# Optimization experiments

Measured on AMD Instinct MI355X. Metric: run time of the kernel, lower is better.

Reference implementation:

```python
import jax, jax.numpy as jnp
import numpy as np

B, C, P, D = 4096, 1000, 10, 256
N = C * P            # total prototypes
E = 160000           # edges among prototypes
MARGIN = -0.1
LOSS_WEIGHT = 0.1
EPS = 1e-12          # F.normalize eps


def _gcn_conv(x, src, dst, deg_isqrt, w, b):
    # PyG GCNConv: symmetric-normalized aggregation with self-loops (added by caller)
    xw = x @ w                                   # [N, D]
    norm = deg_isqrt[src] * deg_isqrt[dst]       # [E+N]
    msg = norm[:, None] * xw[src]                # [E+N, D]
    out = jax.ops.segment_sum(msg, dst, num_segments=N)
    return out + b


def setup_inputs() -> dict:
    key = jax.random.key(0)
    ks = jax.random.split(key, 8)
    return {
        "hidden": jax.random.normal(ks[0], (B, D), jnp.float32),
        "labels": jax.random.randint(ks[1], (B,), 0, C),
        "edge_index": jax.random.randint(ks[2], (2, E), 0, N),
        "node_features": 0.02 * jax.random.normal(ks[3], (N, D), jnp.float32),
        "w1": jax.random.normal(ks[4], (D, D), jnp.float32) / np.sqrt(D),
        "b1": jnp.zeros((D,), jnp.float32),
        "w2": jax.random.normal(ks[5], (D, D), jnp.float32) / np.sqrt(D),
        "b2": jnp.zeros((D,), jnp.float32),
    }


def reference(hidden, labels, edge_index, node_features, w1, b1, w2, b2):
    # --- PrototypeGCN over the prototype graph (self-loops + sym norm) ---
    loops = jnp.arange(N, dtype=edge_index.dtype)
    src = jnp.concatenate([edge_index[0], loops])
    dst = jnp.concatenate([edge_index[1], loops])
    deg = jax.ops.segment_sum(jnp.ones_like(dst, jnp.float32), dst, num_segments=N)
    deg_isqrt = jnp.where(deg > 0, jax.lax.rsqrt(jnp.maximum(deg, 1.0)), 0.0)
    x = node_features
    x = jax.nn.relu(_gcn_conv(x, src, dst, deg_isqrt, w1, b1))
    x = jax.nn.relu(_gcn_conv(x, src, dst, deg_isqrt, w2, b2))

    # --- cosine similarity, per-class max over prototypes ---
    hidden_norm = hidden / jnp.maximum(jnp.linalg.norm(hidden, axis=1, keepdims=True), EPS)
    proto_norm = x / jnp.maximum(jnp.linalg.norm(x, axis=1, keepdims=True), EPS)
    sim = (1.0 + hidden_norm @ proto_norm.T) / 2.0          # [B, N]
    sim_pc = sim.reshape(B, C, P)
    output = sim_pc.max(axis=2)                              # [B, C]
    topk_idx = sim_pc.argmax(axis=2)                         # [B, C]

    # --- margin-masked cross entropy ---
    ar = jnp.arange(B)
    true_scores = output[ar, labels]
    pred_labels = output.argmax(axis=1)
    pred_scores = output.max(axis=1)
    mask = (true_scores - pred_scores) > MARGIN              # [B] bool
    cnt = mask.sum()
    per_ce = -jax.nn.log_softmax(output, axis=1)[ar, labels]
    ce_loss = jnp.sum(per_ce * mask) / jnp.maximum(cnt, 1).astype(per_ce.dtype)

    # dispersion = -mean(proto_norm @ proto_norm.T) = -||sum_i p_i||^2 / N^2
    s = proto_norm.sum(axis=0)
    dispersion_loss = -(s @ s) / (N * N)
    total_loss = jnp.where(cnt == 0, 0.0, ce_loss + LOSS_WEIGHT * dispersion_loss)

    # --- vectorized usage scatter (replaces Python double loop) ---
    pos_ids = labels * P + topk_idx[ar, labels]
    positive_usage = jnp.zeros((N,), jnp.float32).at[pos_ids].add(1.0)
    wrong = (pred_labels != labels).astype(jnp.float32)
    neg_ids = pred_labels * P + topk_idx[ar, pred_labels]
    negative_usage = jnp.zeros((N,), jnp.float32).at[neg_ids].add(wrong)

    return (output, total_loss, positive_usage, negative_usage)
```

## Files before the change

kernel.cpp:

```cpp
#include <hip/hip_runtime.h>
#include <math.h>

#define B_  4096
#define C_  1000
#define P_  10
#define D_  256
#define N_  10000
#define E_  160000

typedef __attribute__((ext_vector_type(8))) short short8;
typedef __attribute__((ext_vector_type(4))) float floatx4;

#define MFMA16(a, b, c) __builtin_amdgcn_mfma_f32_16x16x32_bf16((a), (b), (c), 0, 0, 0)

__device__ __forceinline__ float waveReduceSum(float v){
  #pragma unroll
  for (int o = 32; o > 0; o >>= 1) v += __shfl_xor(v, o);
  return v;
}
__device__ __forceinline__ unsigned short f2bf(float f){
  unsigned int u = __float_as_uint(f);
  unsigned int r = (u + 0x7FFFu + ((u >> 16) & 1u)) >> 16;
  return (unsigned short)r;
}
__device__ __forceinline__ float bf2f(unsigned short b){
  return __uint_as_float(((unsigned int)b) << 16);
}
__device__ __forceinline__ void gload_lds16(const void* g, void* l){
  __builtin_amdgcn_global_load_lds((const __attribute__((address_space(1))) void*)g,
                                   (__attribute__((address_space(3))) void*)l, 16, 0, 0);
}

__global__ void k_prep(const int* __restrict__ src, const int* __restrict__ dst,
                       int* __restrict__ cursor, int* __restrict__ csr_src,
                       const float* __restrict__ w1, const float* __restrict__ w2,
                       unsigned short* __restrict__ w1h, unsigned short* __restrict__ w1l,
                       unsigned short* __restrict__ w2h, unsigned short* __restrict__ w2l,
                       float* __restrict__ zero_zone,
                       const float* __restrict__ nodef,
                       unsigned short* __restrict__ NFh, unsigned short* __restrict__ NFl,
                       const float* __restrict__ hidden,
                       unsigned short* __restrict__ HNh, unsigned short* __restrict__ HNl){
  int b = blockIdx.x;
  int t = threadIdx.x;
  if (b < 625){
    int e = b * 256 + t;
    if (e < E_){
      int d = dst[e];
      int p = atomicAdd(&cursor[d], 1);
      p = (p < 63) ? p : 63;
      csr_src[d * 64 + p] = src[e];
    }
  } else if (b < 1137){
    int bb = b - 625;
    const float* w = (bb < 256) ? w1 : w2;
    int n = bb & 255;
    float x = w[(size_t)t * 256 + n];
    unsigned short h = f2bf(x);
    unsigned short l = f2bf(x - bf2f(h));
    if (bb < 256){ w1h[(size_t)n * 256 + t] = h; w1l[(size_t)n * 256 + t] = l; }
    else         { w2h[(size_t)n * 256 + t] = h; w2l[(size_t)n * 256 + t] = l; }
  } else if (b < 1216){
    int i = (b - 1137) * 256 + t;
    if (i < 1 + 2 * N_) zero_zone[i] = 0.f;
  } else if (b < 11216){
    size_t i = (size_t)(b - 1216) * 256 + t;
    float x = nodef[i];
    unsigned short h = f2bf(x);
    NFh[i] = h;
    NFl[i] = f2bf(x - bf2f(h));
  } else {
    int r = b - 11216;
    float v = hidden[(size_t)r * 256 + t];
    float ss = waveReduceSum(v * v);
    __shared__ float red[4];
    int w = t >> 6;
    if ((t & 63) == 0) red[w] = ss;
    __syncthreads();
    float tot = red[0] + red[1] + red[2] + red[3];
    float nrm = fmaxf(sqrtf(tot), 1e-12f);
    float x = v / nrm;
    unsigned short h = f2bf(x);
    HNh[(size_t)r * 256 + t] = h;
    HNl[(size_t)r * 256 + t] = f2bf(x - bf2f(h));
  }
}

__global__ __launch_bounds__(64) void k_gemm_mfma(
    const unsigned short* __restrict__ Ah, const unsigned short* __restrict__ Al,
    const unsigned short* __restrict__ Wh, const unsigned short* __restrict__ Wl,
    float* __restrict__ outp){
  int lane = threadIdx.x;
  int l15 = lane & 15, lq = lane >> 4;
  int rb = blockIdx.x * 64;
  int nb = blockIdx.y * 32;

  floatx4 acc[4][2];
  #pragma unroll
  for (int mt = 0; mt < 4; ++mt)
    #pragma unroll
    for (int nt = 0; nt < 2; ++nt) acc[mt][nt] = (floatx4){0.f,0.f,0.f,0.f};

  int arow[4];
  #pragma unroll
  for (int mt = 0; mt < 4; ++mt){
    int r = rb + mt * 16 + l15;
    arow[mt] = (r < N_) ? r : (N_ - 1);
  }
  for (int kc = 0; kc < 256; kc += 32){
    short8 ah[4], al[4], bh[2], bl[2];
    #pragma unroll
    for (int mt = 0; mt < 4; ++mt){
      size_t o = (size_t)arow[mt] * 256 + kc + lq * 8;
      ah[mt] = *(const short8*)(Ah + o);
      al[mt] = *(const short8*)(Al + o);
    }
    #pragma unroll
    for (int nt = 0; nt < 2; ++nt){
      size_t o = (size_t)(nb + nt * 16 + l15) * 256 + kc + lq * 8;
      bh[nt] = *(const short8*)(Wh + o);
      bl[nt] = *(const short8*)(Wl + o);
    }
    #pragma unroll
    for (int nt = 0; nt < 2; ++nt)
      #pragma unroll
      for (int mt = 0; mt < 4; ++mt) acc[mt][nt] = MFMA16(al[mt], bh[nt], acc[mt][nt]);
    #pragma unroll
    for (int nt = 0; nt < 2; ++nt)
      #pragma unroll
      for (int mt = 0; mt < 4; ++mt) acc[mt][nt] = MFMA16(ah[mt], bl[nt], acc[mt][nt]);
    #pragma unroll
    for (int nt = 0; nt < 2; ++nt)
      #pragma unroll
      for (int mt = 0; mt < 4; ++mt) acc[mt][nt] = MFMA16(ah[mt], bh[nt], acc[mt][nt]);
  }
  #pragma unroll
  for (int mt = 0; mt < 4; ++mt)
    #pragma unroll
    for (int r = 0; r < 4; ++r){
      int row = rb + mt * 16 + lq * 4 + r;
      if (row < N_){
        #pragma unroll
        for (int nt = 0; nt < 2; ++nt)
          outp[(size_t)row * 256 + nb + nt * 16 + l15] = acc[mt][nt][r];
      }
    }
}

__global__ void k_agg_split(const float* __restrict__ XW, const int* __restrict__ deg,
                            const int* __restrict__ csr_src,
                            const float* __restrict__ bias,
                            unsigned short* __restrict__ Xh, unsigned short* __restrict__ Xl){
  int n    = blockIdx.x * 4 + (threadIdx.x >> 6);
  int lane = threadIdx.x & 63;
  int c4   = lane * 4;
  int dgn = deg[n];
  int dg = (dgn < 64) ? dgn : 64;
  int   esr = (lane < dg) ? csr_src[n * 64 + lane] : 0;
  float is  = 1.0f / sqrtf((float)(dgn + 1));
  float en  = (1.0f / sqrtf((float)(deg[esr] + 1))) * is;
  float4 s = *(const float4*)(XW + (size_t)n * 256 + c4);
  float w = is * is;
  float4 a = make_float4(w * s.x, w * s.y, w * s.z, w * s.w);
  int i = 0;
  for (; i + 3 < dg; i += 4){
    int s0 = __shfl(esr, i),   s1 = __shfl(esr, i+1), s2 = __shfl(esr, i+2), s3 = __shfl(esr, i+3);
    float n0 = __shfl(en, i),  n1 = __shfl(en, i+1),  n2 = __shfl(en, i+2),  n3 = __shfl(en, i+3);
    float4 v0 = *(const float4*)(XW + (size_t)s0 * 256 + c4);
    float4 v1 = *(const float4*)(XW + (size_t)s1 * 256 + c4);
    float4 v2 = *(const float4*)(XW + (size_t)s2 * 256 + c4);
    float4 v3 = *(const float4*)(XW + (size_t)s3 * 256 + c4);
    a.x += n0*v0.x + n1*v1.x + n2*v2.x + n3*v3.x;
    a.y += n0*v0.y + n1*v1.y + n2*v2.y + n3*v3.y;
    a.z += n0*v0.z + n1*v1.z + n2*v2.z + n3*v3.z;
    a.w += n0*v0.w + n1*v1.w + n2*v2.w + n3*v3.w;
  }
  for (; i < dg; ++i){
    int s0 = __shfl(esr, i); float n0 = __shfl(en, i);
    float4 v0 = *(const float4*)(XW + (size_t)s0 * 256 + c4);
    a.x += n0 * v0.x; a.y += n0 * v0.y; a.z += n0 * v0.z; a.w += n0 * v0.w;
  }
  float4 b = *(const float4*)(bias + c4);
  float x0 = fmaxf(a.x + b.x, 0.f), x1 = fmaxf(a.y + b.y, 0.f);
  float x2 = fmaxf(a.z + b.z, 0.f), x3 = fmaxf(a.w + b.w, 0.f);
  unsigned short h0 = f2bf(x0), h1 = f2bf(x1), h2 = f2bf(x2), h3 = f2bf(x3);
  ushort4 hv = make_ushort4(h0, h1, h2, h3);
  ushort4 lv = make_ushort4(f2bf(x0 - bf2f(h0)), f2bf(x1 - bf2f(h1)),
                            f2bf(x2 - bf2f(h2)), f2bf(x3 - bf2f(h3)));
  *(ushort4*)(Xh + (size_t)n * 256 + c4) = hv;
  *(ushort4*)(Xl + (size_t)n * 256 + c4) = lv;
}

__global__ void k_agg_norm_split(const float* __restrict__ XW, const int* __restrict__ deg,
                                 const int* __restrict__ csr_src,
                                 const float* __restrict__ bias,
                                 unsigned short* __restrict__ Ph, unsigned short* __restrict__ Pl){
  int n    = blockIdx.x * 4 + (threadIdx.x >> 6);
  int lane = threadIdx.x & 63;
  int c4   = lane * 4;
  int dgn = deg[n];
  int dg = (dgn < 64) ? dgn : 64;
  int   esr = (lane < dg) ? csr_src[n * 64 + lane] : 0;
  float is  = 1.0f / sqrtf((float)(dgn + 1));
  float en  = (1.0f / sqrtf((float)(deg[esr] + 1))) * is;
  float4 s = *(const float4*)(XW + (size_t)n * 256 + c4);
  float w = is * is;
  float4 a = make_float4(w * s.x, w * s.y, w * s.z, w * s.w);
  int i = 0;
  for (; i + 3 < dg; i += 4){
    int s0 = __shfl(esr, i),   s1 = __shfl(esr, i+1), s2 = __shfl(esr, i+2), s3 = __shfl(esr, i+3);
    float n0 = __shfl(en, i),  n1 = __shfl(en, i+1),  n2 = __shfl(en, i+2),  n3 = __shfl(en, i+3);
    float4 v0 = *(const float4*)(XW + (size_t)s0 * 256 + c4);
    float4 v1 = *(const float4*)(XW + (size_t)s1 * 256 + c4);
    float4 v2 = *(const float4*)(XW + (size_t)s2 * 256 + c4);
    float4 v3 = *(const float4*)(XW + (size_t)s3 * 256 + c4);
    a.x += n0*v0.x + n1*v1.x + n2*v2.x + n3*v3.x;
    a.y += n0*v0.y + n1*v1.y + n2*v2.y + n3*v3.y;
    a.z += n0*v0.z + n1*v1.z + n2*v2.z + n3*v3.z;
    a.w += n0*v0.w + n1*v1.w + n2*v2.w + n3*v3.w;
  }
  for (; i < dg; ++i){
    int s0 = __shfl(esr, i); float n0 = __shfl(en, i);
    float4 v0 = *(const float4*)(XW + (size_t)s0 * 256 + c4);
    a.x += n0 * v0.x; a.y += n0 * v0.y; a.z += n0 * v0.z; a.w += n0 * v0.w;
  }
  float4 b = *(const float4*)(bias + c4);
  float x0 = fmaxf(a.x + b.x, 0.f), x1 = fmaxf(a.y + b.y, 0.f);
  float x2 = fmaxf(a.z + b.z, 0.f), x3 = fmaxf(a.w + b.w, 0.f);
  float ss = x0*x0 + x1*x1 + x2*x2 + x3*x3;
  float tot = waveReduceSum(ss);
  float nrm = fmaxf(sqrtf(tot), 1e-12f);
  x0 /= nrm; x1 /= nrm; x2 /= nrm; x3 /= nrm;
  unsigned short h0 = f2bf(x0), h1 = f2bf(x1), h2 = f2bf(x2), h3 = f2bf(x3);
  ushort4 hv = make_ushort4(h0, h1, h2, h3);
  ushort4 lv = make_ushort4(f2bf(x0 - bf2f(h0)), f2bf(x1 - bf2f(h1)),
                            f2bf(x2 - bf2f(h2)), f2bf(x3 - bf2f(h3)));
  *(ushort4*)(Ph + (size_t)n * 256 + c4) = hv;
  *(ushort4*)(Pl + (size_t)n * 256 + c4) = lv;
}

__global__ __launch_bounds__(256, 4) void k_sim_max(
    const unsigned short* __restrict__ HNh, const unsigned short* __restrict__ HNl,
    const unsigned short* __restrict__ PNh, const unsigned short* __restrict__ PNl,
    float* __restrict__ out, unsigned char* __restrict__ idxb){
  __shared__ __align__(16) char smem[20736];

  int tid  = threadIdx.x;
  int wid  = tid >> 6;
  int lane = tid & 63;
  int l15  = lane & 15, lq = lane >> 4;
  int rbw  = blockIdx.y * 128 + wid * 32;
  int cb80 = blockIdx.x * 80;

  int swz  = (l15 >> 1) & 3;
  int srow = lane >> 2;
  int skq  = (lane & 3) ^ ((lane >> 3) & 3);

  floatx4 acc[2][5];
  #pragma unroll
  for (int mt = 0; mt < 2; ++mt)
    #pragma unroll
    for (int nt = 0; nt < 5; ++nt) acc[mt][nt] = (floatx4){0.f,0.f,0.f,0.f};

  const unsigned short* a0h = HNh + (size_t)(rbw + l15) * 256 + lq * 8;
  const unsigned short* a0l = HNl + (size_t)(rbw + l15) * 256 + lq * 8;

  auto stage1 = [&](int kc, int pb, int c){
    int bsel = (c >= 5) ? 1 : 0;
    int s = c - bsel * 5;
    int row = s * 16 + srow;
    const unsigned short* gp = (bsel ? PNl : PNh)
        + (size_t)(cb80 + row) * 256 + kc + skq * 8;
    char* lp = smem + pb * 10240 + bsel * 5120 + s * 1024;
    gload_lds16(gp, lp);
  };
  auto stageAll = [&](int kc, int pb){
    stage1(kc, pb, wid);
    stage1(kc, pb, wid + 4);
    if (wid < 2) stage1(kc, pb, wid + 8);
  };

  stageAll(0, 0);
  short8 ah[2], al[2];
  #pragma unroll
  for (int mt = 0; mt < 2; ++mt){
    ah[mt] = *(const short8*)(a0h + (size_t)mt * 4096);
    al[mt] = *(const short8*)(a0l + (size_t)mt * 4096);
  }
  __syncthreads();

  int p = 0;
  for (int kc = 0; kc < 256; kc += 32){
    const unsigned short* Bh = (const unsigned short*)(smem + p * 10240);
    const unsigned short* Bl = Bh + 2560;
    short8 ah2[2], al2[2];
    if (kc < 224){
      stageAll(kc + 32, p ^ 1);
      #pragma unroll
      for (int mt = 0; mt < 2; ++mt){
        ah2[mt] = *(const short8*)(a0h + (size_t)mt * 4096 + kc + 32);
        al2[mt] = *(const short8*)(a0l + (size_t)mt * 4096 + kc + 32);
      }
    }
    {
      int r0 = (0 * 16 + l15) * 32 + (lq ^ swz) * 8;
      int r1 = (1 * 16 + l15) * 32 + (lq ^ swz) * 8;
      int r2 = (2 * 16 + l15) * 32 + (lq ^ swz) * 8;
      short8 bh0 = *(const short8*)(Bh + r0), bl0 = *(const short8*)(Bl + r0);
      short8 bh1 = *(const short8*)(Bh + r1), bl1 = *(const short8*)(Bl + r1);
      short8 bh2 = *(const short8*)(Bh + r2), bl2 = *(const short8*)(Bl + r2);
      acc[0][0] = MFMA16(al[0], bh0, acc[0][0]);
      acc[1][0] = MFMA16(al[1], bh0, acc[1][0]);
      acc[0][1] = MFMA16(al[0], bh1, acc[0][1]);
      acc[1][1] = MFMA16(al[1], bh1, acc[1][1]);
      acc[0][2] = MFMA16(al[0], bh2, acc[0][2]);
      acc[1][2] = MFMA16(al[1], bh2, acc[1][2]);
      acc[0][0] = MFMA16(ah[0], bl0, acc[0][0]);
      acc[1][0] = MFMA16(ah[1], bl0, acc[1][0]);
      acc[0][1] = MFMA16(ah[0], bl1, acc[0][1]);
      acc[1][1] = MFMA16(ah[1], bl1, acc[1][1]);
      acc[0][2] = MFMA16(ah[0], bl2, acc[0][2]);
      acc[1][2] = MFMA16(ah[1], bl2, acc[1][2]);
      acc[0][0] = MFMA16(ah[0], bh0, acc[0][0]);
      acc[1][0] = MFMA16(ah[1], bh0, acc[1][0]);
      acc[0][1] = MFMA16(ah[0], bh1, acc[0][1]);
      acc[1][1] = MFMA16(ah[1], bh1, acc[1][1]);
      acc[0][2] = MFMA16(ah[0], bh2, acc[0][2]);
      acc[1][2] = MFMA16(ah[1], bh2, acc[1][2]);
    }
    {
      int r3 = (3 * 16 + l15) * 32 + (lq ^ swz) * 8;
      int r4 = (4 * 16 + l15) * 32 + (lq ^ swz) * 8;
      short8 bh3 = *(const short8*)(Bh + r3), bl3 = *(const short8*)(Bl + r3);
      short8 bh4 = *(const short8*)(Bh + r4), bl4 = *(const short8*)(Bl + r4);
      acc[0][3] = MFMA16(al[0], bh3, acc[0][3]);
      acc[1][3] = MFMA16(al[1], bh3, acc[1][3]);
      acc[0][4] = MFMA16(al[0], bh4, acc[0][4]);
      acc[1][4] = MFMA16(al[1], bh4, acc[1][4]);
      acc[0][3] = MFMA16(ah[0], bl3, acc[0][3]);
      acc[1][3] = MFMA16(ah[1], bl3, acc[1][3]);
      acc[0][4] = MFMA16(ah[0], bl4, acc[0][4]);
      acc[1][4] = MFMA16(ah[1], bl4, acc[1][4]);
      acc[0][3] = MFMA16(ah[0], bh3, acc[0][3]);
      acc[1][3] = MFMA16(ah[1], bh3, acc[1][3]);
      acc[0][4] = MFMA16(ah[0], bh4, acc[0][4]);
      acc[1][4] = MFMA16(ah[1], bh4, acc[1][4]);
    }
    ah[0] = ah2[0]; ah[1] = ah2[1];
    al[0] = al2[0]; al[1] = al2[1];
    __syncthreads();
    p ^= 1;
  }

  float* redw = (float*)smem + wid * 1296;
  #pragma unroll
  for (int mt = 0; mt < 2; ++mt){
    #pragma unroll
    for (int nt = 0; nt < 5; ++nt)
      #pragma unroll
      for (int r = 0; r < 4; ++r)
        redw[(lq * 4 + r) * 81 + nt * 16 + l15] = acc[mt][nt][r];
    int row = lane >> 2;
    int q   = lane & 3;
    const float* basep = redw + row * 81 + q * 20;
    float vs[2]; int is[2];
    #pragma unroll
    for (int cc = 0; cc < 2; ++cc){
      float m = 0.5f * (1.0f + basep[cc * 10]); int mi = 0;
      #pragma unroll
      for (int p2 = 1; p2 < 10; ++p2){
        float v = 0.5f * (1.0f + basep[cc * 10 + p2]);
        if (v > m){ m = v; mi = p2; }
      }
      vs[cc] = m; is[cc] = mi;
    }
    int grow = rbw + mt * 16 + row;
    int gcol = blockIdx.x * 8 + q * 2;
    *(float2*)(out + (size_t)grow * 1000 + gcol) = make_float2(vs[0], vs[1]);
    idxb[(size_t)grow * 1000 + gcol]     = (unsigned char)is[0];
    idxb[(size_t)grow * 1000 + gcol + 1] = (unsigned char)is[1];
  }
}

__global__ void k_row_pass(const float* __restrict__ out, const unsigned char* __restrict__ idxb,
                           const int* __restrict__ labels, int* __restrict__ cnt,
                           float* __restrict__ ce_sum, float* __restrict__ pos_usage,
                           float* __restrict__ neg_usage,
                           const unsigned short* __restrict__ Ph,
                           const unsigned short* __restrict__ Pl,
                           float* __restrict__ svec, int* __restrict__ done,
                           float* __restrict__ loss_out){
  int blk = blockIdx.x;
  if (blk < 1024){
    int b = blk * 4 + (threadIdx.x >> 6);
    int lane = threadIdx.x & 63;
    const float* row = out + (size_t)b * 1000;
    float m = -INFINITY, s = 0.f; int bi = 0x7fffffff;
    for (int c = lane; c < 1000; c += 64){
      float v = row[c];
      if (v > m){ s = s * expf(m - v) + 1.f; bi = c; m = v; }
      else       s += expf(v - m);
    }
    #pragma unroll
    for (int o = 32; o > 0; o >>= 1){
      float m2 = __shfl_xor(m, o);
      float s2 = __shfl_xor(s, o);
      int   b2 = __shfl_xor(bi, o);
      float M = fmaxf(m, m2);
      s = s * expf(m - M) + s2 * expf(m2 - M);
      if (m2 > m || (m2 == m && b2 < bi)) bi = b2;
      m = M;
    }
    if (lane == 0){
      int lab = labels[b];
      float true_score = row[lab];
      float per_ce = m + logf(s) - true_score;
      bool mask = (true_score - m) > -0.1f;
      if (mask){ atomicAdd(cnt, 1); atomicAdd(ce_sum, per_ce); }
      int pi = idxb[(size_t)b * 1000 + lab];
      atomicAdd(&pos_usage[lab * P_ + pi], 1.f);
      if (bi != lab){
        int ni = idxb[(size_t)b * 1000 + bi];
        atomicAdd(&neg_usage[bi * P_ + ni], 1.f);
      }
    }
  } else {
    int t = threadIdx.x;
    int r0 = (blk - 1024) * 100;
    float acc = 0.f;
    for (int rr = r0; rr < r0 + 100; ++rr)
      acc += bf2f(Ph[(size_t)rr * 256 + t]) + bf2f(Pl[(size_t)rr * 256 + t]);
    atomicAdd(&svec[t], acc);
  }
  __threadfence();
  __syncthreads();
  __shared__ int last;
  if (threadIdx.x == 0){
    int d = atomicAdd(done, 1);
    last = (d == 1124 - 1) ? 1 : 0;
  }
  __syncthreads();
  if (last){
    __threadfence();
    int t = threadIdx.x;
    float v = atomicAdd(&svec[t], 0.f);
    float ss = waveReduceSum(v * v);
    __shared__ float red[4];
    if ((t & 63) == 0) red[t >> 6] = ss;
    __syncthreads();
    if (t == 0){
      float tot = red[0] + red[1] + red[2] + red[3];
      float disp = -tot / 1.0e8f;
      int c = atomicAdd(cnt, 0);
      float ces = atomicAdd(ce_sum, 0.f);
      float total = (c == 0) ? 0.f
                  : (ces / (float)(c < 1 ? 1 : c) + 0.1f * disp);
      *loss_out = total;
    }
  }
}

extern "C" void kernel_launch(void* const* d_in, const int* in_sizes, int n_in,
                              void* d_out, int out_size, void* d_ws, size_t ws_size,
                              hipStream_t stream){
  const float* hidden = (const float*)d_in[0];
  const int*   labels = (const int*)  d_in[1];
  const int*   eidx   = (const int*)  d_in[2];
  const float* nodef  = (const float*)d_in[3];
  const float* w1     = (const float*)d_in[4];
  const float* b1     = (const float*)d_in[5];
  const float* w2     = (const float*)d_in[6];
  const float* b2     = (const float*)d_in[7];

  float* out       = (float*)d_out;
  float* loss_out  = out + (size_t)B_ * C_;
  float* pos_usage = loss_out + 1;
  float* neg_usage = pos_usage + N_;

  const int* srcp = eidx;
  const int* dstp = eidx + E_;

  char* base = (char*)d_ws;
  size_t off = 0;
  auto alloc = [&](size_t bytes) -> char* {
    char* p = base + off;
    off = (off + bytes + 255) & ~(size_t)255;
    return p;
  };
  int*   cursor  = (int*)  alloc((size_t)N_ * 4);
  float* svec    = (float*)alloc(256 * 4);
  int*   cnt     = (int*)  alloc(4);
  float* ce_sum  = (float*)alloc(4);
  int*   done    = (int*)  alloc(4);
  size_t zero_bytes = off;
  int*   csr_src   = (int*)  alloc((size_t)N_ * 64 * 4);
  float* XW        = (float*)alloc((size_t)N_ * 256 * 4);
  unsigned short* NFh = (unsigned short*)alloc((size_t)N_ * 256 * 2);
  unsigned short* NFl = (unsigned short*)alloc((size_t)N_ * 256 * 2);
  unsigned short* Xh  = (unsigned short*)alloc((size_t)N_ * 256 * 2);
  unsigned short* Xl  = (unsigned short*)alloc((size_t)N_ * 256 * 2);
  unsigned short* Ph  = (unsigned short*)alloc((size_t)N_ * 256 * 2);
  unsigned short* Pl  = (unsigned short*)alloc((size_t)N_ * 256 * 2);
  unsigned short* W1h = (unsigned short*)alloc(256 * 256 * 2);
  unsigned short* W1l = (unsigned short*)alloc(256 * 256 * 2);
  unsigned short* W2h = (unsigned short*)alloc(256 * 256 * 2);
  unsigned short* W2l = (unsigned short*)alloc(256 * 256 * 2);
  unsigned short* HNh = (unsigned short*)alloc((size_t)B_ * 256 * 2);
  unsigned short* HNl = (unsigned short*)alloc((size_t)B_ * 256 * 2);
  unsigned char* idxb = (unsigned char*)alloc((size_t)B_ * C_);

  hipMemsetAsync(base, 0, zero_bytes, stream);

  k_prep<<<15312, 256, 0, stream>>>(srcp, dstp, cursor, csr_src,
                                    w1, w2, W1h, W1l, W2h, W2l, loss_out,
                                    nodef, NFh, NFl, hidden, HNh, HNl);

  dim3 ggrid(157, 8);
  k_gemm_mfma<<<ggrid, 64, 0, stream>>>(NFh, NFl, W1h, W1l, XW);
  k_agg_split<<<N_ / 4, 256, 0, stream>>>(XW, cursor, csr_src, b1, Xh, Xl);
  k_gemm_mfma<<<ggrid, 64, 0, stream>>>(Xh, Xl, W2h, W2l, XW);
  k_agg_norm_split<<<N_ / 4, 256, 0, stream>>>(XW, cursor, csr_src, b2, Ph, Pl);

  dim3 sgrid(125, 32);
  k_sim_max<<<sgrid, 256, 0, stream>>>(HNh, HNl, Ph, Pl, out, idxb);

  k_row_pass<<<1124, 256, 0, stream>>>(out, idxb, labels, cnt, ce_sum,
                                       pos_usage, neg_usage, Ph, Pl, svec, done, loss_out);
}
```

Baseline: 383.3 us.

## Split row pass: separate colsum and finalize kernels, vectorize row max/softmax

Moves the prototype column-sum into its own kernel launched before the similarity kernel. Replaces the last-block completion counter with a separate single-block finalize kernel. Rewrites the per-row pass to load the row with float4 into registers, find max/argmax first, then compute the exp sum with fast intrinsics instead of the serial online softmax. Adds two kernel launches, and the fast exp/log intrinsics may slightly change numerics.

```diff
diff --git a/kernel.cpp b/kernel.cpp
--- a/kernel.cpp
+++ b/kernel.cpp
@@ -239,6 +239,17 @@
   *(ushort4*)(Pl + (size_t)n * 256 + c4) = lv;
 }
 
+__global__ void k_colsum(const unsigned short* __restrict__ hi,
+                         const unsigned short* __restrict__ lo,
+                         float* __restrict__ s){
+  int d = threadIdx.x;
+  int r0 = blockIdx.x * 100;
+  float acc = 0.f;
+  for (int r = r0; r < r0 + 100; ++r)
+    acc += bf2f(hi[(size_t)r * 256 + d]) + bf2f(lo[(size_t)r * 256 + d]);
+  atomicAdd(&s[d], acc);
+}
+
 __global__ __launch_bounds__(256, 4) void k_sim_max(
     const unsigned short* __restrict__ HNh, const unsigned short* __restrict__ HNl,
     const unsigned short* __restrict__ PNh, const unsigned short* __restrict__ PNl,
@@ -385,78 +396,69 @@
 __global__ void k_row_pass(const float* __restrict__ out, const unsigned char* __restrict__ idxb,
                            const int* __restrict__ labels, int* __restrict__ cnt,
                            float* __restrict__ ce_sum, float* __restrict__ pos_usage,
-                           float* __restrict__ neg_usage,
-                           const unsigned short* __restrict__ Ph,
-                           const unsigned short* __restrict__ Pl,
-                           float* __restrict__ svec, int* __restrict__ done,
-                           float* __restrict__ loss_out){
-  int blk = blockIdx.x;
-  if (blk < 1024){
-    int b = blk * 4 + (threadIdx.x >> 6);
-    int lane = threadIdx.x & 63;
-    const float* row = out + (size_t)b * 1000;
-    float m = -INFINITY, s = 0.f; int bi = 0x7fffffff;
-    for (int c = lane; c < 1000; c += 64){
-      float v = row[c];
-      if (v > m){ s = s * expf(m - v) + 1.f; bi = c; m = v; }
-      else       s += expf(v - m);
-    }
-    #pragma unroll
-    for (int o = 32; o > 0; o >>= 1){
-      float m2 = __shfl_xor(m, o);
-      float s2 = __shfl_xor(s, o);
-      int   b2 = __shfl_xor(bi, o);
-      float M = fmaxf(m, m2);
-      s = s * expf(m - M) + s2 * expf(m2 - M);
-      if (m2 > m || (m2 == m && b2 < bi)) bi = b2;
-      m = M;
-    }
-    if (lane == 0){
-      int lab = labels[b];
-      float true_score = row[lab];
-      float per_ce = m + logf(s) - true_score;
-      bool mask = (true_score - m) > -0.1f;
-      if (mask){ atomicAdd(cnt, 1); atomicAdd(ce_sum, per_ce); }
-      int pi = idxb[(size_t)b * 1000 + lab];
-      atomicAdd(&pos_usage[lab * P_ + pi], 1.f);
-      if (bi != lab){
-        int ni = idxb[(size_t)b * 1000 + bi];
-        atomicAdd(&neg_usage[bi * P_ + ni], 1.f);
-      }
-    }
-  } else {
-    int t = threadIdx.x;
-    int r0 = (blk - 1024) * 100;
-    float acc = 0.f;
-    for (int rr = r0; rr < r0 + 100; ++rr)
-      acc += bf2f(Ph[(size_t)rr * 256 + t]) + bf2f(Pl[(size_t)rr * 256 + t]);
-    atomicAdd(&svec[t], acc);
-  }
-  __threadfence();
+                           float* __restrict__ neg_usage){
+  int b = blockIdx.x * 4 + (threadIdx.x >> 6);
+  int lane = threadIdx.x & 63;
+  const float* row = out + (size_t)b * 1000;
+  float v[16];
+  #pragma unroll
+  for (int j = 0; j < 4; ++j){
+    int f4 = j * 64 + lane;
+    if (f4 < 250){
+      float4 t = *(const float4*)(row + f4 * 4);
+      v[j*4+0] = t.x; v[j*4+1] = t.y; v[j*4+2] = t.z; v[j*4+3] = t.w;
+    } else {
+      v[j*4+0] = v[j*4+1] = v[j*4+2] = v[j*4+3] = -INFINITY;
+    }
+  }
+  float m = -INFINITY; int mi = 0x7fffffff;
+  #pragma unroll
+  for (int j = 0; j < 4; ++j)
+    #pragma unroll
+    for (int k = 0; k < 4; ++k){
+      float x = v[j*4+k];
+      if (x > m){ m = x; mi = (j * 64 + lane) * 4 + k; }
+    }
+  #pragma unroll
+  for (int o = 32; o > 0; o >>= 1){
+    float m2 = __shfl_xor(m, o);
+    int   i2 = __shfl_xor(mi, o);
+    if (m2 > m || (m2 == m && i2 < mi)){ m = m2; mi = i2; }
+  }
+  float s = 0.f;
+  #pragma unroll
+  for (int t = 0; t < 16; ++t) s += __expf(v[t] - m);
+  s = waveReduceSum(s);
+  if (lane == 0){
+    int lab = labels[b];
+    float true_score = row[lab];
+    float per_ce = m + __logf(s) - true_score;
+    bool mask = (true_score - m) > -0.1f;
+    if (mask){ atomicAdd(cnt, 1); atomicAdd(ce_sum, per_ce); }
+    int pi = idxb[(size_t)b * 1000 + lab];
+    atomicAdd(&pos_usage[lab * P_ + pi], 1.f);
+    if (mi != lab){
+      int ni = idxb[(size_t)b * 1000 + mi];
+      atomicAdd(&neg_usage[mi * P_ + ni], 1.f);
+    }
+  }
+}
+
+__global__ void k_finalize(const float* __restrict__ s, const int* __restrict__ cnt,
+                           const float* __restrict__ ce_sum, float* __restrict__ loss_out){
+  int t = threadIdx.x;
+  float v = s[t];
+  float ss = waveReduceSum(v * v);
+  __shared__ float red[4];
+  if ((t & 63) == 0) red[t >> 6] = ss;
   __syncthreads();
-  __shared__ int last;
-  if (threadIdx.x == 0){
-    int d = atomicAdd(done, 1);
-    last = (d == 1124 - 1) ? 1 : 0;
-  }
-  __syncthreads();
-  if (last){
-    __threadfence();
-    int t = threadIdx.x;
-    float v = atomicAdd(&svec[t], 0.f);
-    float ss = waveReduceSum(v * v);
-    __shared__ float red[4];
-    if ((t & 63) == 0) red[t >> 6] = ss;
-    __syncthreads();
-    if (t == 0){
-      float tot = red[0] + red[1] + red[2] + red[3];
-      float disp = -tot / 1.0e8f;
-      int c = atomicAdd(cnt, 0);
-      float ces = atomicAdd(ce_sum, 0.f);
-      float total = (c == 0) ? 0.f
-                  : (ces / (float)(c < 1 ? 1 : c) + 0.1f * disp);
-      *loss_out = total;
-    }
+  if (t == 0){
+    float tot = red[0] + red[1] + red[2] + red[3];
+    float disp = -tot / 1.0e8f;
+    int c = *cnt;
+    float total = (c == 0) ? 0.f
+                : (*ce_sum / (float)(c < 1 ? 1 : c) + 0.1f * disp);
+    *loss_out = total;
   }
 }
 
@@ -491,7 +493,6 @@
   float* svec    = (float*)alloc(256 * 4);
   int*   cnt     = (int*)  alloc(4);
   float* ce_sum  = (float*)alloc(4);
-  int*   done    = (int*)  alloc(4);
   size_t zero_bytes = off;
   int*   csr_src   = (int*)  alloc((size_t)N_ * 64 * 4);
   float* XW        = (float*)alloc((size_t)N_ * 256 * 4);
@@ -521,9 +522,11 @@
   k_gemm_mfma<<<ggrid, 64, 0, stream>>>(Xh, Xl, W2h, W2l, XW);
   k_agg_norm_split<<<N_ / 4, 256, 0, stream>>>(XW, cursor, csr_src, b2, Ph, Pl);
 
+  k_colsum<<<100, 256, 0, stream>>>(Ph, Pl, svec);
+
   dim3 sgrid(125, 32);
   k_sim_max<<<sgrid, 256, 0, stream>>>(HNh, HNl, Ph, Pl, out, idxb);
 
-  k_row_pass<<<1124, 256, 0, stream>>>(out, idxb, labels, cnt, ce_sum,
-                                       pos_usage, neg_usage, Ph, Pl, svec, done, loss_out);
-}
+  k_row_pass<<<B_ / 4, 256, 0, stream>>>(out, idxb, labels, cnt, ce_sum, pos_usage, neg_usage);
+  k_finalize<<<1, 256, 0, stream>>>(svec, cnt, ce_sum, loss_out);
+}
```

New measurement: 334.3 us. 1.15x faster.
